# Kernel optimization log

Hardware: AMD Instinct MI355X
Metric: run time of the kernel (lower is better)

The kernel has to match this reference:

```python
import jax, jax.numpy as jnp
import numpy as np

B = 512      # streamlines (graphs in the batch)
L = 128      # points per streamline
M = L - 1    # edges per direction per streamline == conv output length
IN = 3       # 3-D coordinates
K = 5        # kNN neighbors (self included, as in PyG knn)
FOV = 5      # conv kernel; odd so conv out length == M, matching the batch vector
PAD = FOV // 2
NC = 2
EPS = 1e-5


def _bn(x, g, b, m, v):
    # inference-mode BatchNorm1d
    return (x - m) * jax.lax.rsqrt(v + EPS) * g + b


def setup_inputs():
    key = jax.random.key(0)
    ks = jax.random.split(key, 20)
    r = lambda i, shape: jax.random.normal(ks[i], shape, jnp.float32) * 0.05
    ones = lambda n: jnp.ones((n,), jnp.float32)
    zeros = lambda n: jnp.zeros((n,), jnp.float32)
    pos = jax.random.normal(ks[0], (B * L, IN), jnp.float32)
    # consecutive-point (forward) edges, streamline-major order
    base = (jnp.arange(B)[:, None] * L + jnp.arange(M)[None, :]).reshape(-1)
    fwd = jnp.stack([base, base + 1]).astype(jnp.int32)          # [2, B*M]
    eidx = jnp.concatenate([fwd, fwd], axis=1)                   # [2, 2*B*M]; first half overwritten in forward
    batch = jnp.repeat(jnp.arange(B, dtype=jnp.int32), L)        # per-point graph id
    lengths = jnp.full((B,), L, dtype=jnp.int32)
    return dict(
        pos=pos, eidx=eidx, batch=batch, lengths=lengths,
        conv1_w=r(1, (FOV, 2 * IN, 64)), conv1_b=r(2, (64,)),
        bn1_g=ones(64), bn1_b=zeros(64), bn1_m=r(3, (64,)), bn1_v=ones(64),
        edge_w=r(4, (2 * 64, 128)), edge_b=r(5, (128,)),
        bn2_g=ones(128), bn2_b=zeros(128), bn2_m=r(6, (128,)), bn2_v=ones(128),
        lin1_w=r(7, (64 + 128, 1024)), lin1_b=r(8, (1024,)),
        bn3_g=ones(1024), bn3_b=zeros(1024), bn3_m=r(9, (1024,)), bn3_v=ones(1024),
        m1_w=r(10, (1024, 512)), m1_b=r(11, (512,)),
        bn4_g=ones(512), bn4_b=zeros(512), bn4_m=r(12, (512,)), bn4_v=ones(512),
        m2_w=r(13, (512, 256)), m2_b=r(14, (256,)),
        bn5_g=ones(256), bn5_b=zeros(256), bn5_m=r(15, (256,)), bn5_v=ones(256),
        out_w=r(16, (256, NC)), out_b=r(17, (NC,)),
    )


def reference(pos, eidx, batch, lengths,
              conv1_w, conv1_b, bn1_g, bn1_b, bn1_m, bn1_v,
              edge_w, edge_b, bn2_g, bn2_b, bn2_m, bn2_v,
              lin1_w, lin1_b, bn3_g, bn3_b, bn3_m, bn3_v,
              m1_w, m1_b, bn4_g, bn4_b, bn4_m, bn4_v,
              m2_w, m2_b, bn5_g, bn5_b, bn5_m, bn5_v,
              out_w, out_b):
    E = eidx.shape[1]
    half = eidx[:, E // 2:]
    # eidx[:, :E//2] = eidx[:, E//2:].flip(1)
    eidx = jnp.concatenate([half[:, ::-1], half], axis=1)
    # irregular gather: edge features [E, 2*IN]
    feats = jnp.concatenate([pos[eidx[1]] - pos[eidx[0]], pos[eidx[0]]], axis=1)
    x = feats.reshape(2 * B, M, 2 * IN)                            # folded direction+batch
    # Conv1d (cross-correlation) -> BN -> ReLU, channels-last layout
    x = jax.lax.conv_general_dilated(x, conv1_w, (1,), [(PAD, PAD)],
                                     dimension_numbers=('NWC', 'WIO', 'NWC')) + conv1_b
    x = jax.nn.relu(_bn(x, bn1_g, bn1_b, bn1_m, bn1_v))            # [2B, M, 64]
    # direction symmetrization: max(first half, second half flipped on batch & length)
    x = jnp.maximum(x[:B], x[B:][::-1, ::-1, :])                   # [B, M, 64]
    x1 = x.reshape(B * M, 64)
    # ---- DynamicEdgeConv: per-streamline kNN graph + edge MLP + max aggregation ----
    xg = x1.reshape(B, M, 64)
    sq = jnp.sum(xg * xg, axis=-1)                                 # [B, M]
    dist = sq[:, :, None] + sq[:, None, :] - 2.0 * jnp.einsum('bmd,bnd->bmn', xg, xg)
    _, idx = jax.lax.top_k(-dist, K)                               # [B, M, K] (self included)
    xj = jax.vmap(lambda xs, ix: xs[ix])(xg, idx)                  # [B, M, K, 64]
    xi = jnp.broadcast_to(xg[:, :, None, :], xj.shape)
    ef = jnp.concatenate([xi, xj - xi], axis=-1)                   # [B, M, K, 128]
    ef = _bn(jax.nn.relu(ef @ edge_w + edge_b), bn2_g, bn2_b, bn2_m, bn2_v)
    x2 = jnp.max(ef, axis=2).reshape(B * M, 128)                   # max aggr over neighbors
    # ---- lin1 + global max pool + classifier MLP (dropout = identity in eval) ----
    h = jnp.concatenate([x1, x2], axis=1)                          # [N, 192]
    h = _bn(jax.nn.relu(h @ lin1_w + lin1_b), bn3_g, bn3_b, bn3_m, bn3_v)  # [N, 1024]
    g = jnp.max(h.reshape(B, M, 1024), axis=1)                     # global_max_pool -> [B, 1024]
    g = _bn(jax.nn.relu(g @ m1_w + m1_b), bn4_g, bn4_b, bn4_m, bn4_v)
    g = _bn(jax.nn.relu(g @ m2_w + m2_b), bn5_g, bn5_b, bn5_m, bn5_v)
    return g @ out_w + out_b                                       # [B, NC]
```

## Files before the change

### kernel.cpp

```cpp
#include <hip/hip_runtime.h>

#define BB 512
#define LL 128
#define MM 127
#define EPS 1e-5f

typedef _Float16 half4 __attribute__((ext_vector_type(4)));
typedef _Float16 half8 __attribute__((ext_vector_type(8)));
typedef float f32x16 __attribute__((ext_vector_type(16)));

#define HB_PITCH 384
#define HB_BATCH 49152

__global__ __launch_bounds__(256) void k0_prep(
    const float* __restrict__ lw, char* __restrict__ lwT,
    const float* __restrict__ ew, char* __restrict__ ewT,
    const float* __restrict__ m1w, char* __restrict__ m1wT,
    const float* __restrict__ m2w, char* __restrict__ m2wT)
{
  int tid = threadIdx.x;
  __shared__ float ws2[256][32];
  if (blockIdx.x < 32) {
    int c0 = blockIdx.x * 32;
    __shared__ float wcol[192][32];
    for (int i = tid; i < 192 * 32; i += 256) {
      int k = i >> 5, c = i & 31;
      wcol[k][c] = lw[k * 1024 + c0 + c];
    }
    __syncthreads();
    for (int j = tid; j < 768; j += 256) {
      int kg = j >> 5, c = j & 31;
      half8 v;
#pragma unroll
      for (int jj = 0; jj < 8; jj++) v[jj] = (_Float16)wcol[kg * 8 + jj][c];
      int cc = c0 + c;
      *(half8*)(lwT + cc * HB_PITCH + ((kg * 16) ^ ((cc & 7) << 4))) = v;
    }
  } else if (blockIdx.x == 32) {
    __shared__ float es[128][128];
    for (int i = tid; i < 128 * 128; i += 256) es[i >> 7][i & 127] = ew[i];
    __syncthreads();
    for (int i = tid; i < 256 * 8; i += 256) {
      int c = i >> 3, kg = i & 7;
      half8 v;
#pragma unroll
      for (int jj = 0; jj < 8; jj++) {
        int k = kg * 8 + jj;
        float val = (c < 128) ? (es[k][c] - es[64 + k][c]) : es[64 + k][c - 128];
        v[jj] = (_Float16)val;
      }
      *(half8*)(ewT + c * 128 + ((kg * 16) ^ ((c & 7) << 4))) = v;
    }
  } else {
    const float* src; char* dst; int N, K, c0, k0;
    if (blockIdx.x < 97) {
      int bb = blockIdx.x - 33;
      src = m1w; dst = m1wT; N = 512; K = 1024;
      c0 = (bb >> 2) * 32; k0 = (bb & 3) * 256;
    } else {
      int bb = blockIdx.x - 97;
      src = m2w; dst = m2wT; N = 256; K = 512;
      c0 = (bb >> 1) * 32; k0 = (bb & 1) * 256;
    }
    for (int i = tid; i < 256 * 32; i += 256) {
      int k = i >> 5, c = i & 31;
      ws2[k][c] = src[(size_t)(k0 + k) * N + c0 + c];
    }
    __syncthreads();
    for (int j = tid; j < 32 * 32; j += 256) {
      int kg = j >> 5, c = j & 31;
      half8 v;
#pragma unroll
      for (int jj = 0; jj < 8; jj++) v[jj] = (_Float16)ws2[kg * 8 + jj][c];
      int cc = c0 + c;
      *(half8*)(dst + (size_t)cc * (2 * K) + ((2 * (k0 + kg * 8)) ^ ((cc & 7) << 4))) = v;
    }
  }
}

__global__ __launch_bounds__(256) void k1_conv(
    const float* __restrict__ pos, const float* __restrict__ cw,
    const float* __restrict__ cb, const float* __restrict__ g1,
    const float* __restrict__ b1, const float* __restrict__ m1,
    const float* __restrict__ v1, float* __restrict__ xg,
    char* __restrict__ hb)
{
  int b = blockIdx.x;
  int tid = threadIdx.x;
  __shared__ float ps[LL * 3];
  __shared__ float fpad[MM + 4][6];
  __shared__ float ws[5 * 6 * 64];
  __shared__ float s1s[64], t1s[64];
  for (int i = tid; i < LL * 3; i += 256) ps[i] = pos[b * LL * 3 + i];
  for (int i = tid; i < 5 * 6 * 64; i += 256) ws[i] = cw[i];
  if (tid < 64) {
    float s = g1[tid] * rsqrtf(v1[tid] + EPS);
    s1s[tid] = s;
    t1s[tid] = (cb[tid] - m1[tid]) * s + b1[tid];
  }
  if (tid < 24) {
    int r = tid / 6, c = tid % 6;
    int rr = (r < 2) ? r : (MM + r);
    fpad[rr][c] = 0.f;
  }
  __syncthreads();
  for (int i = tid; i < MM * 6; i += 256) {
    int m = i / 6, c = i % 6;
    float v = (c < 3) ? (ps[(m + 1) * 3 + c] - ps[m * 3 + c]) : ps[m * 3 + c - 3];
    fpad[m + 2][c] = v;
  }
  __syncthreads();
  int orow = BB - 1 - b;
  char* hbb = hb + (size_t)orow * HB_BATCH;
  if (tid < 8) *(float4*)(hbb + 127 * HB_PITCH + tid * 16) = make_float4(0.f, 0.f, 0.f, 0.f);
  for (int o = tid; o < MM * 64; o += 256) {
    int m = o >> 6, c = o & 63;
    float af = 0.f, ab = 0.f;
#pragma unroll
    for (int t = 0; t < 5; t++) {
#pragma unroll
      for (int ci = 0; ci < 6; ci++) {
        float wv = ws[(t * 6 + ci) * 64 + c];
        af = fmaf(fpad[m + t][ci], wv, af);
        ab = fmaf(fpad[m + 4 - t][ci], wv, ab);
      }
    }
    float z = fmaxf(af, ab) * s1s[c] + t1s[c];
    float xv = fmaxf(z, 0.f);
    int p = MM - 1 - m;
    xg[(orow * MM + p) * 64 + c] = xv;
    *(_Float16*)(hbb + p * HB_PITCH + ((2 * c) ^ ((p & 7) << 4))) = (_Float16)xv;
  }
}

__global__ __launch_bounds__(256) void k2_knn(
    const float* __restrict__ xg, int* __restrict__ idxb)
{
  int b = blockIdx.x;
  int tid = threadIdx.x;
  int g = tid >> 7, row = tid & 127;
  __shared__ float4 xs4[MM][16];
  __shared__ float sq[MM];
  __shared__ float bsl[2][128][5];
  __shared__ int   bil[2][128][5];
  const float4* src = (const float4*)(xg + b * MM * 64);
  for (int i = tid; i < MM * 16; i += 256) xs4[i >> 4][i & 15] = src[i];
  __syncthreads();
  float4 xm4[16];
  if (row < MM) {
    float s = 0.f;
#pragma unroll
    for (int d4 = 0; d4 < 16; d4++) {
      xm4[d4] = xs4[row][d4];
      s = fmaf(xm4[d4].x, xm4[d4].x, s);
      s = fmaf(xm4[d4].y, xm4[d4].y, s);
      s = fmaf(xm4[d4].z, xm4[d4].z, s);
      s = fmaf(xm4[d4].w, xm4[d4].w, s);
    }
    if (g == 0) sq[row] = s;
  }
  __syncthreads();
  float bs[5]; int bi[5];
#pragma unroll
  for (int k = 0; k < 5; k++) { bs[k] = 1e30f; bi[k] = 0; }
  if (row < MM) {
    int j0 = g * 64;
    int j1 = g ? MM : 64;
    for (int j = j0; j < j1; j++) {
      float dot = 0.f;
#pragma unroll
      for (int d4 = 0; d4 < 16; d4++) {
        float4 xv = xs4[j][d4];
        dot = fmaf(xm4[d4].x, xv.x, dot);
        dot = fmaf(xm4[d4].y, xv.y, dot);
        dot = fmaf(xm4[d4].z, xv.z, dot);
        dot = fmaf(xm4[d4].w, xv.w, dot);
      }
      float sc = sq[j] - 2.f * dot;
      if (sc < bs[4]) {
        bs[4] = sc; bi[4] = j;
#pragma unroll
        for (int k = 3; k >= 0; k--) {
          if (bs[k + 1] < bs[k]) {
            float ts = bs[k]; bs[k] = bs[k + 1]; bs[k + 1] = ts;
            int ti = bi[k]; bi[k] = bi[k + 1]; bi[k + 1] = ti;
          }
        }
      }
    }
  }
#pragma unroll
  for (int k = 0; k < 5; k++) { bsl[g][row][k] = bs[k]; bil[g][row][k] = bi[k]; }
  __syncthreads();
  if (tid < MM) {
    int i0 = 0, i1 = 0;
    int base = (b * MM + tid) * 5;
#pragma unroll
    for (int k = 0; k < 5; k++) {
      float v0 = bsl[0][tid][i0], v1 = bsl[1][tid][i1];
      int id;
      if (v0 <= v1) { id = bil[0][tid][i0]; i0++; }
      else          { id = bil[1][tid][i1]; i1++; }
      idxb[base + k] = id;
    }
  }
}

__global__ __launch_bounds__(256) void k3_edge(
    const int* __restrict__ idxb, const char* __restrict__ ewT,
    const float* __restrict__ eb, const float* __restrict__ g2,
    const float* __restrict__ b2, const float* __restrict__ m2,
    const float* __restrict__ v2, char* __restrict__ hb)
{
  int b = blockIdx.x;
  int tid = threadIdx.x;
  int w = tid >> 6, l = tid & 63;
  int lo = l & 31, hi = l >> 5;
  __shared__ _Float16 vvs[MM][136];
  __shared__ int idxs[MM * 5];
  char* hbb = hb + (size_t)b * HB_BATCH;

  for (int i = tid; i < MM * 5; i += 256) idxs[i] = idxb[b * MM * 5 + i];
  if (tid < 16) *(float4*)(hbb + 127 * HB_PITCH + 128 + tid * 16) = make_float4(0.f, 0.f, 0.f, 0.f);

  half8 af[4][4];
#pragma unroll
  for (int rt = 0; rt < 4; rt++) {
    int row = rt * 32 + lo;
    const char* rb = hbb + row * HB_PITCH;
    int sz = (row & 7) << 4;
#pragma unroll
    for (int ks = 0; ks < 4; ks++)
      af[rt][ks] = *(const half8*)(rb + ((ks * 32 + hi * 16) ^ sz));
  }
  int cu = w * 32 + lo;
  int swzW = (cu & 7) << 4;
  const char* wu = ewT + cu * 128;
  const char* wv = ewT + (128 + cu) * 128;
  half8 bu[4], bv[4];
#pragma unroll
  for (int ks = 0; ks < 4; ks++) {
    int off = (ks * 32 + hi * 16) ^ swzW;
    bu[ks] = *(const half8*)(wu + off);
    bv[ks] = *(const half8*)(wv + off);
  }
  f32x16 accu[4], accv[4];
#pragma unroll
  for (int rt = 0; rt < 4; rt++)
#pragma unroll
    for (int r = 0; r < 16; r++) { accu[rt][r] = 0.f; accv[rt][r] = 0.f; }
#pragma unroll
  for (int ks = 0; ks < 4; ks++)
#pragma unroll
    for (int rt = 0; rt < 4; rt++) {
      accu[rt] = __builtin_amdgcn_mfma_f32_32x32x16_f16(af[rt][ks], bu[ks], accu[rt], 0, 0, 0);
      accv[rt] = __builtin_amdgcn_mfma_f32_32x32x16_f16(af[rt][ks], bv[ks], accv[rt], 0, 0, 0);
    }
#pragma unroll
  for (int rt = 0; rt < 4; rt++)
#pragma unroll
    for (int r = 0; r < 16; r++) {
      int p = rt * 32 + (r & 3) + 8 * (r >> 2) + 4 * hi;
      if (p < MM) vvs[p][cu] = (_Float16)accv[rt][r];
    }
  __syncthreads();
  float ebv = eb[cu];
  float s2 = g2[cu] * rsqrtf(v2[cu] + EPS);
  float t2 = b2[cu] - m2[cu] * s2;
#pragma unroll
  for (int rt = 0; rt < 4; rt++)
#pragma unroll
    for (int r = 0; r < 16; r++) {
      int p = rt * 32 + (r & 3) + 8 * (r >> 2) + 4 * hi;
      if (p >= MM) continue;
      const int* ip = &idxs[p * 5];
      float u = accu[rt][r];
      float mx = -1e30f;
#pragma unroll
      for (int k = 0; k < 5; k++)
        mx = fmaxf(mx, u + (float)vvs[ip[k]][cu]);
      float o = fmaxf(mx + ebv, 0.f) * s2 + t2;
      *(_Float16*)(hbb + p * HB_PITCH + ((128 + 2 * cu) ^ ((p & 7) << 4))) = (_Float16)o;
    }
}

__global__ __launch_bounds__(512, 2) void k4_lin1(
    const char* __restrict__ hb, const char* __restrict__ lwT,
    const float* __restrict__ lb, const float* __restrict__ g3,
    const float* __restrict__ b3, const float* __restrict__ m3,
    const float* __restrict__ v3, char* __restrict__ gbufh)
{
  int b = blockIdx.x;
  int tid = threadIdx.x;
  int w = tid >> 6;
  int rh = w >> 2, cq = w & 3;
  int l = tid & 63;
  int lo = l & 31, hi = l >> 5;
  __shared__ __align__(16) char sA[HB_BATCH];
  __shared__ float rmslab[2][1024];

  {
    const char* gA = hb + (size_t)b * HB_BATCH;
#pragma unroll
    for (int i = 0; i < 6; i++)
      *(float4*)(sA + (i * 512 + tid) * 16) = *(const float4*)(gA + (i * 512 + tid) * 16);
  }
  __syncthreads();

  int sz = (lo & 7) << 4;
  half8 af[2][12];
#pragma unroll
  for (int q = 0; q < 2; q++) {
    const char* rbase = sA + ((rh * 2 + q) * 32 + lo) * HB_PITCH;
#pragma unroll
    for (int ks = 0; ks < 12; ks++)
      af[q][ks] = *(const half8*)(rbase + ((ks * 32 + hi * 16) ^ sz));
  }

  int col0 = cq * 256 + lo;
  half8 bf[2][12];
  {
    const char* cb0 = lwT + (size_t)col0 * HB_PITCH;
#pragma unroll
    for (int ks = 0; ks < 12; ks++)
      bf[0][ks] = *(const half8*)(cb0 + ((ks * 32 + hi * 16) ^ sz));
  }
#pragma unroll
  for (int ct = 0; ct < 8; ct++) {
    if (ct < 7) {
      const char* cbn = lwT + (size_t)(col0 + (ct + 1) * 32) * HB_PITCH;
#pragma unroll
      for (int ks = 0; ks < 12; ks++)
        bf[(ct + 1) & 1][ks] = *(const half8*)(cbn + ((ks * 32 + hi * 16) ^ sz));
    }
    f32x16 acc[2];
#pragma unroll
    for (int q = 0; q < 2; q++)
#pragma unroll
      for (int r = 0; r < 16; r++) acc[q][r] = 0.f;
#pragma unroll
    for (int ks = 0; ks < 12; ks++) {
      acc[0] = __builtin_amdgcn_mfma_f32_32x32x16_f16(af[0][ks], bf[ct & 1][ks], acc[0], 0, 0, 0);
      acc[1] = __builtin_amdgcn_mfma_f32_32x32x16_f16(af[1][ks], bf[ct & 1][ks], acc[1], 0, 0, 0);
    }
    int col = col0 + ct * 32;
    float bias = lb[col];
    float rm = 0.f;
#pragma unroll
    for (int q = 0; q < 2; q++)
#pragma unroll
      for (int r = 0; r < 16; r++) {
        float v = fmaxf(acc[q][r] + bias, 0.f);
        if (q == 1 && r == 15) v = (rh == 1 && hi == 1) ? 0.f : v;
        rm = fmaxf(rm, v);
      }
    rm = fmaxf(rm, __shfl_xor(rm, 32));
    if (hi == 0) rmslab[rh][col] = rm;
  }
  __syncthreads();
  if (tid < 256) {
    half4 o;
#pragma unroll
    for (int j = 0; j < 4; j++) {
      int c = tid * 4 + j;
      float mv = fmaxf(rmslab[0][c], rmslab[1][c]);
      float s = g3[c] * rsqrtf(v3[c] + EPS);
      float t = b3[c] - m3[c] * s;
      o[j] = (_Float16)(mv * s + t);
    }
    *(half4*)(gbufh + (size_t)b * 2048 + ((8 * tid) ^ ((b & 7) << 4))) = o;
  }
}

template<int K, int N>
__global__ __launch_bounds__(64) void k5_gemm(
    const char* __restrict__ inh, const char* __restrict__ wT,
    const float* __restrict__ bias, const float* __restrict__ gg,
    const float* __restrict__ bbp, const float* __restrict__ mmp,
    const float* __restrict__ vvp, char* __restrict__ outh,
    float* __restrict__ outf)
{
  constexpr int NT = N / 32;
  constexpr int NC = K / 128;
  int bid = blockIdx.x;
  int mt = bid / NT, nt = bid % NT;
  int l = threadIdx.x;
  int lo = l & 31, hi = l >> 5;
  int row = mt * 32 + lo, col = nt * 32 + lo;
  const char* arow = inh + (size_t)row * (2 * K);
  const char* brow = wT + (size_t)col * (2 * K);
  int sza = (row & 7) << 4, szb = (col & 7) << 4;

  half8 a[2][8], bf[2][8];
#pragma unroll
  for (int ks = 0; ks < 8; ks++) {
    int off = ks * 32 + hi * 16;
    a[0][ks]  = *(const half8*)(arow + (off ^ sza));
    bf[0][ks] = *(const half8*)(brow + (off ^ szb));
  }
  f32x16 acc;
#pragma unroll
  for (int r = 0; r < 16; r++) acc[r] = 0.f;
#pragma unroll
  for (int c = 0; c < NC; c++) {
    if (c + 1 < NC) {
#pragma unroll
      for (int ks = 0; ks < 8; ks++) {
        int off = (c + 1) * 256 + ks * 32 + hi * 16;
        a[(c + 1) & 1][ks]  = *(const half8*)(arow + (off ^ sza));
        bf[(c + 1) & 1][ks] = *(const half8*)(brow + (off ^ szb));
      }
    }
#pragma unroll
    for (int ks = 0; ks < 8; ks++)
      acc = __builtin_amdgcn_mfma_f32_32x32x16_f16(a[c & 1][ks], bf[c & 1][ks], acc, 0, 0, 0);
  }
  float bv = bias[col];
  float s = gg[col] * rsqrtf(vvp[col] + EPS);
  float t = bbp[col] - mmp[col] * s;
#pragma unroll
  for (int r = 0; r < 16; r++) {
    float z = fmaxf(acc[r] + bv, 0.f) * s + t;
    int orow = mt * 32 + (r & 3) + 8 * (r >> 2) + 4 * hi;
    if (outh)
      *(_Float16*)(outh + (size_t)orow * (2 * N) + ((2 * col) ^ ((orow & 7) << 4))) = (_Float16)z;
    else
      outf[(size_t)orow * N + col] = z;
  }
}

__global__ __launch_bounds__(256) void k5c_out(
    const float* __restrict__ c2, const float* __restrict__ ow,
    const float* __restrict__ ob, float* __restrict__ out)
{
  int t = blockIdx.x * 256 + threadIdx.x;
  int r = t >> 1, c = t & 1;
  float acc = 0.f;
  for (int d4 = 0; d4 < 64; d4++) {
    float4 cv = *(const float4*)(c2 + r * 256 + d4 * 4);
    acc = fmaf(cv.x, ow[(d4 * 4 + 0) * 2 + c], acc);
    acc = fmaf(cv.y, ow[(d4 * 4 + 1) * 2 + c], acc);
    acc = fmaf(cv.z, ow[(d4 * 4 + 2) * 2 + c], acc);
    acc = fmaf(cv.w, ow[(d4 * 4 + 3) * 2 + c], acc);
  }
  out[t] = acc + ob[c];
}

extern "C" void kernel_launch(void* const* d_in, const int* in_sizes, int n_in,
                              void* d_out, int out_size, void* d_ws, size_t ws_size,
                              hipStream_t stream)
{
  const float* pos = (const float*)d_in[0];
  const float* cw  = (const float*)d_in[4];
  const float* cb  = (const float*)d_in[5];
  const float* g1  = (const float*)d_in[6];
  const float* b1  = (const float*)d_in[7];
  const float* m1  = (const float*)d_in[8];
  const float* v1  = (const float*)d_in[9];
  const float* ew  = (const float*)d_in[10];
  const float* eb  = (const float*)d_in[11];
  const float* g2  = (const float*)d_in[12];
  const float* b2  = (const float*)d_in[13];
  const float* m2  = (const float*)d_in[14];
  const float* v2  = (const float*)d_in[15];
  const float* lw  = (const float*)d_in[16];
  const float* lb  = (const float*)d_in[17];
  const float* g3  = (const float*)d_in[18];
  const float* b3  = (const float*)d_in[19];
  const float* m3  = (const float*)d_in[20];
  const float* v3  = (const float*)d_in[21];
  const float* m1w = (const float*)d_in[22];
  const float* m1b = (const float*)d_in[23];
  const float* g4  = (const float*)d_in[24];
  const float* b4  = (const float*)d_in[25];
  const float* m4  = (const float*)d_in[26];
  const float* v4  = (const float*)d_in[27];
  const float* m2w = (const float*)d_in[28];
  const float* m2b = (const float*)d_in[29];
  const float* g5  = (const float*)d_in[30];
  const float* b5  = (const float*)d_in[31];
  const float* m5  = (const float*)d_in[32];
  const float* v5  = (const float*)d_in[33];
  const float* ow  = (const float*)d_in[34];
  const float* ob  = (const float*)d_in[35];

  char* ws = (char*)d_ws;
  float* xg    = (float*)(ws);
  char*  hb    = ws + 16646144;
  char*  lwT   = ws + 41811968;
  char*  ewT   = ws + 42205184;
  int*   idxb  = (int*)(ws + 42237952);
  char*  gbufh = ws + 43538432;
  char*  m1wT  = ws + 44587008;
  char*  c1h   = ws + 45635584;
  char*  m2wT  = ws + 46159872;
  float* c2    = (float*)(ws + 46422016);

  hipLaunchKernelGGL(k0_prep, dim3(113), dim3(256), 0, stream,
                     lw, lwT, ew, ewT, m1w, m1wT, m2w, m2wT);
  hipLaunchKernelGGL(k1_conv, dim3(512), dim3(256), 0, stream,
                     pos, cw, cb, g1, b1, m1, v1, xg, hb);
  hipLaunchKernelGGL(k2_knn, dim3(512), dim3(256), 0, stream, xg, idxb);
  hipLaunchKernelGGL(k3_edge, dim3(512), dim3(256), 0, stream,
                     idxb, ewT, eb, g2, b2, m2, v2, hb);
  hipLaunchKernelGGL(k4_lin1, dim3(512), dim3(512), 0, stream,
                     hb, lwT, lb, g3, b3, m3, v3, gbufh);
  (k5_gemm<1024, 512>)<<<dim3(256), dim3(64), 0, stream>>>(
      gbufh, m1wT, m1b, g4, b4, m4, v4, c1h, nullptr);
  (k5_gemm<512, 256>)<<<dim3(128), dim3(64), 0, stream>>>(
      c1h, m2wT, m2b, g5, b5, m5, v5, nullptr, c2);
  hipLaunchKernelGGL(k5c_out, dim3(4), dim3(256), 0, stream,
                     c2, ow, ob, (float*)d_out);
}
```

Before: 133.8 us.

## Fuse conv and kNN kernels with register-tiled distance matrix in shared memory

Merges the conv kernel and the kNN kernel into one, so conv features stay in LDS instead of being written to and re-read from a global fp32 buffer. The pairwise dot products are now computed as an 8x8 register-tiled GEMM into a shared distance matrix, which is then scanned for the top-5. This removes one launch and the global round trip for xg, and raises arithmetic intensity of the distance step. In exchange the kernel uses much more shared memory (about 120KB, with launch_bounds(256,1)), which lowers occupancy.

```diff
diff --git a/kernel.cpp b/kernel.cpp
--- a/kernel.cpp
+++ b/kernel.cpp
@@ -78,12 +78,12 @@
   }
 }
 
-__global__ __launch_bounds__(256) void k1_conv(
+__global__ __launch_bounds__(256, 1) void k1_conv_knn(
     const float* __restrict__ pos, const float* __restrict__ cw,
     const float* __restrict__ cb, const float* __restrict__ g1,
     const float* __restrict__ b1, const float* __restrict__ m1,
-    const float* __restrict__ v1, float* __restrict__ xg,
-    char* __restrict__ hb)
+    const float* __restrict__ v1, char* __restrict__ hb,
+    int* __restrict__ idxb)
 {
   int b = blockIdx.x;
   int tid = threadIdx.x;
@@ -91,6 +91,12 @@
   __shared__ float fpad[MM + 4][6];
   __shared__ float ws[5 * 6 * 64];
   __shared__ float s1s[64], t1s[64];
+  __shared__ float xs[128][64];
+  __shared__ float sq[128];
+  __shared__ float S[128][132];
+  __shared__ float bsl[2][128][5];
+  __shared__ int   bil[2][128][5];
+
   for (int i = tid; i < LL * 3; i += 256) ps[i] = pos[b * LL * 3 + i];
   for (int i = tid; i < 5 * 6 * 64; i += 256) ws[i] = cw[i];
   if (tid < 64) {
@@ -103,6 +109,7 @@
     int rr = (r < 2) ? r : (MM + r);
     fpad[rr][c] = 0.f;
   }
+  if (tid < 64) xs[127][tid] = 0.f;
   __syncthreads();
   for (int i = tid; i < MM * 6; i += 256) {
     int m = i / 6, c = i % 6;
@@ -128,73 +135,94 @@
     float z = fmaxf(af, ab) * s1s[c] + t1s[c];
     float xv = fmaxf(z, 0.f);
     int p = MM - 1 - m;
-    xg[(orow * MM + p) * 64 + c] = xv;
+    xs[p][(((c >> 2) + (p >> 3)) & 15) * 4 + (c & 3)] = xv;
     *(_Float16*)(hbb + p * HB_PITCH + ((2 * c) ^ ((p & 7) << 4))) = (_Float16)xv;
   }
-}
-
-__global__ __launch_bounds__(256) void k2_knn(
-    const float* __restrict__ xg, int* __restrict__ idxb)
-{
-  int b = blockIdx.x;
-  int tid = threadIdx.x;
-  int g = tid >> 7, row = tid & 127;
-  __shared__ float4 xs4[MM][16];
-  __shared__ float sq[MM];
-  __shared__ float bsl[2][128][5];
-  __shared__ int   bil[2][128][5];
-  const float4* src = (const float4*)(xg + b * MM * 64);
-  for (int i = tid; i < MM * 16; i += 256) xs4[i >> 4][i & 15] = src[i];
-  __syncthreads();
-  float4 xm4[16];
-  if (row < MM) {
+  __syncthreads();
+  if (tid < 128) {
+    int r = tid;
     float s = 0.f;
 #pragma unroll
-    for (int d4 = 0; d4 < 16; d4++) {
-      xm4[d4] = xs4[row][d4];
-      s = fmaf(xm4[d4].x, xm4[d4].x, s);
-      s = fmaf(xm4[d4].y, xm4[d4].y, s);
-      s = fmaf(xm4[d4].z, xm4[d4].z, s);
-      s = fmaf(xm4[d4].w, xm4[d4].w, s);
-    }
-    if (g == 0) sq[row] = s;
-  }
-  __syncthreads();
-  float bs[5]; int bi[5];
-#pragma unroll
-  for (int k = 0; k < 5; k++) { bs[k] = 1e30f; bi[k] = 0; }
-  if (row < MM) {
-    int j0 = g * 64;
-    int j1 = g ? MM : 64;
-    for (int j = j0; j < j1; j++) {
-      float dot = 0.f;
-#pragma unroll
-      for (int d4 = 0; d4 < 16; d4++) {
-        float4 xv = xs4[j][d4];
-        dot = fmaf(xm4[d4].x, xv.x, dot);
-        dot = fmaf(xm4[d4].y, xv.y, dot);
-        dot = fmaf(xm4[d4].z, xv.z, dot);
-        dot = fmaf(xm4[d4].w, xv.w, dot);
-      }
-      float sc = sq[j] - 2.f * dot;
-      if (sc < bs[4]) {
-        bs[4] = sc; bi[4] = j;
-#pragma unroll
-        for (int k = 3; k >= 0; k--) {
-          if (bs[k + 1] < bs[k]) {
-            float ts = bs[k]; bs[k] = bs[k + 1]; bs[k + 1] = ts;
-            int ti = bi[k]; bi[k] = bi[k + 1]; bi[k + 1] = ti;
+    for (int c4 = 0; c4 < 16; c4++) {
+      float4 v = *(const float4*)&xs[r][((c4 + (r >> 3)) & 15) * 4];
+      s = fmaf(v.x, v.x, s); s = fmaf(v.y, v.y, s);
+      s = fmaf(v.z, v.z, s); s = fmaf(v.w, v.w, s);
+    }
+    sq[r] = s;
+  }
+  __syncthreads();
+  {
+    int tr = tid >> 4, tc = tid & 15;
+    float acc[8][8];
+#pragma unroll
+    for (int i = 0; i < 8; i++)
+#pragma unroll
+      for (int j = 0; j < 8; j++) acc[i][j] = 0.f;
+    for (int k4 = 0; k4 < 16; k4++) {
+      int ca = ((k4 + tr) & 15) * 4;
+      int cbo = ((k4 + tc) & 15) * 4;
+      float4 av[8], bv[8];
+#pragma unroll
+      for (int i = 0; i < 8; i++) av[i] = *(const float4*)&xs[tr * 8 + i][ca];
+#pragma unroll
+      for (int j = 0; j < 8; j++) bv[j] = *(const float4*)&xs[tc * 8 + j][cbo];
+#pragma unroll
+      for (int i = 0; i < 8; i++)
+#pragma unroll
+        for (int j = 0; j < 8; j++) {
+          acc[i][j] = fmaf(av[i].x, bv[j].x, acc[i][j]);
+          acc[i][j] = fmaf(av[i].y, bv[j].y, acc[i][j]);
+          acc[i][j] = fmaf(av[i].z, bv[j].z, acc[i][j]);
+          acc[i][j] = fmaf(av[i].w, bv[j].w, acc[i][j]);
+        }
+    }
+    float sqc[8];
+#pragma unroll
+    for (int j = 0; j < 8; j++) sqc[j] = sq[tc * 8 + j];
+#pragma unroll
+    for (int i = 0; i < 8; i++) {
+      float4 s0, s1;
+      s0.x = sqc[0] - 2.f * acc[i][0]; s0.y = sqc[1] - 2.f * acc[i][1];
+      s0.z = sqc[2] - 2.f * acc[i][2]; s0.w = sqc[3] - 2.f * acc[i][3];
+      s1.x = sqc[4] - 2.f * acc[i][4]; s1.y = sqc[5] - 2.f * acc[i][5];
+      s1.z = sqc[6] - 2.f * acc[i][6]; s1.w = sqc[7] - 2.f * acc[i][7];
+      *(float4*)&S[tr * 8 + i][tc * 8]     = s0;
+      *(float4*)&S[tr * 8 + i][tc * 8 + 4] = s1;
+    }
+  }
+  __syncthreads();
+  {
+    int row = tid & 127, half = tid >> 7;
+    float bs[5]; int bi[5];
+#pragma unroll
+    for (int k = 0; k < 5; k++) { bs[k] = 1e30f; bi[k] = 0; }
+    for (int q = 0; q < 16; q++) {
+      float4 sv = *(const float4*)&S[row][half * 64 + q * 4];
+      int cbase = half * 64 + q * 4;
+      float va[4] = {sv.x, sv.y, sv.z, sv.w};
+#pragma unroll
+      for (int e = 0; e < 4; e++) {
+        int col = cbase + e;
+        float sc = va[e];
+        if (col < 127 && sc < bs[4]) {
+          bs[4] = sc; bi[4] = col;
+#pragma unroll
+          for (int k = 3; k >= 0; k--) {
+            if (bs[k + 1] < bs[k]) {
+              float ts = bs[k]; bs[k] = bs[k + 1]; bs[k + 1] = ts;
+              int ti = bi[k]; bi[k] = bi[k + 1]; bi[k + 1] = ti;
+            }
           }
         }
       }
     }
-  }
-#pragma unroll
-  for (int k = 0; k < 5; k++) { bsl[g][row][k] = bs[k]; bil[g][row][k] = bi[k]; }
+#pragma unroll
+    for (int k = 0; k < 5; k++) { bsl[half][row][k] = bs[k]; bil[half][row][k] = bi[k]; }
+  }
   __syncthreads();
   if (tid < MM) {
     int i0 = 0, i1 = 0;
-    int base = (b * MM + tid) * 5;
+    int base = (orow * MM + tid) * 5;
 #pragma unroll
     for (int k = 0; k < 5; k++) {
       float v0 = bsl[0][tid][i0], v1 = bsl[1][tid][i1];
@@ -485,22 +513,20 @@
   const float* ob  = (const float*)d_in[35];
 
   char* ws = (char*)d_ws;
-  float* xg    = (float*)(ws);
-  char*  hb    = ws + 16646144;
-  char*  lwT   = ws + 41811968;
-  char*  ewT   = ws + 42205184;
-  int*   idxb  = (int*)(ws + 42237952);
-  char*  gbufh = ws + 43538432;
-  char*  m1wT  = ws + 44587008;
-  char*  c1h   = ws + 45635584;
-  char*  m2wT  = ws + 46159872;
-  float* c2    = (float*)(ws + 46422016);
+  char*  hb    = ws;
+  char*  lwT   = ws + 25165824;
+  char*  ewT   = ws + 25559040;
+  int*   idxb  = (int*)(ws + 25591808);
+  char*  gbufh = ws + 26892288;
+  char*  m1wT  = ws + 27940864;
+  char*  c1h   = ws + 28989440;
+  char*  m2wT  = ws + 29513728;
+  float* c2    = (float*)(ws + 29775872);
 
   hipLaunchKernelGGL(k0_prep, dim3(113), dim3(256), 0, stream,
                      lw, lwT, ew, ewT, m1w, m1wT, m2w, m2wT);
-  hipLaunchKernelGGL(k1_conv, dim3(512), dim3(256), 0, stream,
-                     pos, cw, cb, g1, b1, m1, v1, xg, hb);
-  hipLaunchKernelGGL(k2_knn, dim3(512), dim3(256), 0, stream, xg, idxb);
+  hipLaunchKernelGGL(k1_conv_knn, dim3(512), dim3(256), 0, stream,
+                     pos, cw, cb, g1, b1, m1, v1, hb, idxb);
   hipLaunchKernelGGL(k3_edge, dim3(512), dim3(256), 0, stream,
                      idxb, ewT, eb, g2, b2, m2, v2, hb);
   hipLaunchKernelGGL(k4_lin1, dim3(512), dim3(512), 0, stream,
```

Result: slower. 140.3 us (+4.9%).
